# Kernel optimization log

Hardware: AMD Instinct MI355X
Metric: run time of the kernel (lower is better)

The kernel has to match this reference:

```python
import jax, jax.numpy as jnp
import numpy as np

B, T, C = 2, 2048, 1024
H, HS = 16, 64          # num_heads, head_size; H*HS == C
FF = 4 * C
EPS = 1e-5


def setup_inputs() -> dict:
    key = jax.random.key(0)
    ks = jax.random.split(key, 10)
    s = 0.02
    return {
        "x": jax.random.normal(ks[0], (B, T, C), dtype=jnp.float32),
        "Wq": jax.random.normal(ks[1], (H, C, HS), dtype=jnp.float32) * s,
        "Wk": jax.random.normal(ks[2], (H, C, HS), dtype=jnp.float32) * s,
        "Wv": jax.random.normal(ks[3], (H, C, HS), dtype=jnp.float32) * s,
        "p": jnp.ones((H,), dtype=jnp.float32),  # per-head learnable scale, init 1
        "Wproj": jax.random.normal(ks[4], (C, C), dtype=jnp.float32) * s,
        "W1": jax.random.normal(ks[5], (C, FF), dtype=jnp.float32) * s,
        "W2": jax.random.normal(ks[6], (FF, C), dtype=jnp.float32) * s,
        "ln1_w": jnp.ones((C,), dtype=jnp.float32),
        "ln1_b": jnp.zeros((C,), dtype=jnp.float32),
        "ln2_w": jnp.ones((C,), dtype=jnp.float32),
        "ln2_b": jnp.zeros((C,), dtype=jnp.float32),
    }


def _layernorm(x, w, b):
    mu = jnp.mean(x, axis=-1, keepdims=True)
    var = jnp.mean(jnp.square(x - mu), axis=-1, keepdims=True)
    return (x - mu) * jax.lax.rsqrt(var + EPS) * w + b


def reference(x, Wq, Wk, Wv, p, Wproj, W1, W2, ln1_w, ln1_b, ln2_w, ln2_b):
    # --- multi-head causal self-attention (dropout p=0 -> identity) ---
    h = _layernorm(x, ln1_w, ln1_b)
    q = jnp.einsum("btc,hcs->bhts", h, Wq)  # [B,H,T,HS]
    k = jnp.einsum("btc,hcs->bhts", h, Wk)
    v = jnp.einsum("btc,hcs->bhts", h, Wv)
    scale = p ** (-0.5)  # per-head scale, p init to 1
    wei = jnp.einsum("bhts,bhks->bhtk", q, k) * scale[None, :, None, None]
    causal = jnp.tril(jnp.ones((T, T), dtype=bool))
    wei = jnp.where(causal[None, None], wei, -jnp.inf)
    wei = jax.nn.softmax(wei, axis=-1)
    att = jnp.einsum("bhtk,bhks->bhts", wei, v)          # [B,H,T,HS]
    att = att.transpose(0, 2, 1, 3).reshape(B, T, C)     # concat heads
    sa = att @ Wproj
    x = x + sa
    # --- feed-forward (activation_id=0 -> ReLU) ---
    h2 = _layernorm(x, ln2_w, ln2_b)
    ff = jax.nn.relu(h2 @ W1) @ W2
    return x + ff
```

## Files before the change

### kernel.cpp

```cpp
#include <hip/hip_runtime.h>


typedef _Float16 f16;
typedef _Float16 f16x8 __attribute__((ext_vector_type(8)));
typedef _Float16 f16x4v __attribute__((ext_vector_type(4)));
typedef float f32x4 __attribute__((ext_vector_type(4)));

static constexpr int Tn = 2048;
static constexpr int Cn = 1024;
static constexpr int HSn = 64;

__device__ __forceinline__ void glds16(const f16* g, f16* l) {
    __builtin_amdgcn_global_load_lds((const __attribute__((address_space(1))) void*)g,
                                     (__attribute__((address_space(3))) void*)l,
                                     16, 0, 0);
}

#define VMCNT(N) asm volatile("s_waitcnt vmcnt(" #N ")" ::: "memory")
__device__ __forceinline__ void barrier_raw() {
    asm volatile("" ::: "memory");
    __builtin_amdgcn_s_barrier();
    asm volatile("" ::: "memory");
}

__device__ __forceinline__ unsigned cvt_pk_u32(float a, float b) {
    auto v = __builtin_amdgcn_cvt_pkrtz(a, b);
    union { __fp16 h2 __attribute__((ext_vector_type(2))); unsigned u; } c;
    c.h2 = v;
    return c.u;
}

__global__ __launch_bounds__(256) void ln_kernel(const float* __restrict__ x,
                                                 const float* __restrict__ w,
                                                 const float* __restrict__ b,
                                                 f16* __restrict__ out) {
    int row = blockIdx.x;
    const float* xr = x + (size_t)row * Cn;
    int tid = threadIdx.x, l = tid & 63, wv = tid >> 6;
    float4 v = *(const float4*)(xr + tid * 4);
    float s = v.x + v.y + v.z + v.w;
    float sq = v.x * v.x + v.y * v.y + v.z * v.z + v.w * v.w;
#pragma unroll
    for (int off = 32; off > 0; off >>= 1) {
        s += __shfl_down(s, off);
        sq += __shfl_down(sq, off);
    }
    __shared__ float red[8];
    if (l == 0) { red[wv] = s; red[wv + 4] = sq; }
    __syncthreads();
    float ts = red[0] + red[1] + red[2] + red[3];
    float tq = red[4] + red[5] + red[6] + red[7];
    float mean = ts * (1.0f / Cn);
    float var = tq * (1.0f / Cn) - mean * mean;
    float rstd = rsqrtf(var + 1e-5f);
    float4 wv4 = *(const float4*)(w + tid * 4);
    float4 bv4 = *(const float4*)(b + tid * 4);
    f16x4v o;
    o[0] = (f16)((v.x - mean) * rstd * wv4.x + bv4.x);
    o[1] = (f16)((v.y - mean) * rstd * wv4.y + bv4.y);
    o[2] = (f16)((v.z - mean) * rstd * wv4.z + bv4.z);
    o[3] = (f16)((v.w - mean) * rstd * wv4.w + bv4.w);
    *(f16x4v*)(out + (size_t)row * Cn + tid * 4) = o;
}

__global__ __launch_bounds__(256) void tr_cast_f32(const float* __restrict__ in, int irs,
                                                   f16* __restrict__ out, int ors) {
    __shared__ float tile[32][33];
    int r0 = blockIdx.x * 32, c0 = blockIdx.y * 32;
    int t = threadIdx.x;
    int rr = t >> 3, c4 = (t & 7) * 4;
    float4 v = *(const float4*)(in + (size_t)(r0 + rr) * irs + c0 + c4);
    tile[rr][c4] = v.x; tile[rr][c4 + 1] = v.y; tile[rr][c4 + 2] = v.z; tile[rr][c4 + 3] = v.w;
    __syncthreads();
    int cc = t >> 3, r4 = (t & 7) * 4;
    f16x4v o;
    o[0] = (f16)tile[r4][cc];
    o[1] = (f16)tile[r4 + 1][cc];
    o[2] = (f16)tile[r4 + 2][cc];
    o[3] = (f16)tile[r4 + 3][cc];
    *(f16x4v*)(out + (size_t)(c0 + cc) * ors + r0 + r4) = o;
}

__global__ __launch_bounds__(256) void tr_cast_qkv(const float* __restrict__ Wq,
                                                   const float* __restrict__ Wk,
                                                   const float* __restrict__ Wv,
                                                   f16* __restrict__ out) {
    int z = blockIdx.z;
    int qkv = z >> 4, h = z & 15;
    const float* in = (qkv == 0 ? Wq : qkv == 1 ? Wk : Wv) + (size_t)h * Cn * HSn;
    f16* o = out + (size_t)(qkv * Cn + h * HSn) * Cn;
    __shared__ float tile[32][33];
    int r0 = blockIdx.x * 32, c0 = blockIdx.y * 32;
    int t = threadIdx.x;
    int rr = t >> 3, c4 = (t & 7) * 4;
    float4 v = *(const float4*)(in + (size_t)(r0 + rr) * HSn + c0 + c4);
    tile[rr][c4] = v.x; tile[rr][c4 + 1] = v.y; tile[rr][c4 + 2] = v.z; tile[rr][c4 + 3] = v.w;
    __syncthreads();
    int cc = t >> 3, r4 = (t & 7) * 4;
    f16x4v ov;
    ov[0] = (f16)tile[r4][cc];
    ov[1] = (f16)tile[r4 + 1][cc];
    ov[2] = (f16)tile[r4 + 2][cc];
    ov[3] = (f16)tile[r4 + 3][cc];
    *(f16x4v*)(o + (size_t)(c0 + cc) * Cn + r0 + r4) = ov;
}

__global__ __launch_bounds__(256) void tr_vT(const f16* __restrict__ QKV, f16* __restrict__ vT) {
    int bh = blockIdx.z;
    int b = bh >> 4, h = bh & 15;
    const f16* in = QKV + (size_t)b * Tn * 3072 + 2048 + h * HSn;
    f16* out = vT + (size_t)bh * HSn * Tn;
    int r0 = blockIdx.x * 64;
    __shared__ __align__(16) f16 tile[64][72];
    int t = threadIdx.x;
#pragma unroll
    for (int i = 0; i < 2; i++) {
        int f = i * 256 + t;
        int rr = f >> 3, c8 = (f & 7) * 8;
        *(uint4*)(&tile[rr][c8]) = *(const uint4*)(in + (size_t)(r0 + rr) * 3072 + c8);
    }
    __syncthreads();
#pragma unroll
    for (int i = 0; i < 2; i++) {
        int f = i * 256 + t;
        int cc = f >> 3, r8 = (f & 7) * 8;
        union { f16 h[8]; uint4 v; } u;
#pragma unroll
        for (int j = 0; j < 8; j++) u.h[j] = tile[r8 + j][cc];
        *(uint4*)(out + (size_t)cc * Tn + r0 + r8) = u.v;
    }
}

template <int EPI>
__global__ __launch_bounds__(512, 2) void gemm8(const f16* __restrict__ A, const f16* __restrict__ Bt,
                                                f16* __restrict__ Cout, int M, int N, int K) {
    __shared__ __align__(16) f16 Abuf[4][8192];
    __shared__ __align__(16) f16 Bbuf[4][8192];
    int wg = blockIdx.x;
    int xcd = wg & 7, idx = wg >> 3;
    int bm = xcd * 2 + (idx & 1), bn = idx >> 1;
    int tid = threadIdx.x, l = tid & 63, w = tid >> 6;
    int wr = w >> 2, wc = w & 3;

    f32x4 acc[8][4];
#pragma unroll
    for (int m = 0; m < 8; m++)
#pragma unroll
        for (int n = 0; n < 4; n++) acc[m][n] = f32x4{0.f, 0.f, 0.f, 0.f};

    int l15 = l & 15;
    int lane_off = l15 * 32 + (((l >> 4) ^ ((l15 >> 1) & 3)) << 3);
    const f16* Afr = &Abuf[0][wr * 4096 + lane_off];
    const f16* Bfr = &Bbuf[0][(wc >> 1) * 4096 + (wc & 1) * 2048 + lane_off];

    int srow = w * 16 + (l >> 2);
    int schunk = (l & 3) ^ ((l >> 3) & 3);
    const f16* agp = A + (size_t)(bm * 256 + srow) * K + schunk * 8;
    const f16* bgp = Bt + (size_t)(bn * 256 + srow) * K + schunk * 8;
    const size_t rK = (size_t)128 * K;
    f16* dstA = &Abuf[0][w * 512];
    f16* dstB = &Bbuf[0][w * 512];

    auto stage = [&](int kt, int bf) {
        int k0 = kt * 32;
        glds16(agp + k0, dstA + bf * 8192);
        glds16(agp + rK + k0, dstA + bf * 8192 + 4096);
        glds16(bgp + k0, dstB + bf * 8192);
        glds16(bgp + rK + k0, dstB + bf * 8192 + 4096);
    };

    int NT = K >> 5;
    stage(0, 0);
    stage(1, 1);
    stage(2, 2);
    for (int t = 0; t < NT; ++t) {
        int cb = t & 3;
        VMCNT(8);
        barrier_raw();
        const f16* Ab = Afr + cb * 8192;
        const f16* Bb = Bfr + cb * 8192;
        f16x8 af[4], bf4[4];
#pragma unroll
        for (int m = 0; m < 4; m++) af[m] = *(const f16x8*)(Ab + m * 512);
#pragma unroll
        for (int n = 0; n < 4; n++) bf4[n] = *(const f16x8*)(Bb + n * 512);
        if (t + 3 < NT) stage(t + 3, (t + 3) & 3);
        __builtin_amdgcn_s_setprio(1);
#pragma unroll
        for (int m = 0; m < 4; m++)
#pragma unroll
            for (int n = 0; n < 4; n++)
                acc[m][n] = __builtin_amdgcn_mfma_f32_16x16x32_f16(af[m], bf4[n], acc[m][n], 0, 0, 0);
        __builtin_amdgcn_s_setprio(0);
        barrier_raw();
#pragma unroll
        for (int m = 0; m < 4; m++) af[m] = *(const f16x8*)(Ab + (m + 4) * 512);
        __builtin_amdgcn_s_setprio(1);
#pragma unroll
        for (int m = 0; m < 4; m++)
#pragma unroll
            for (int n = 0; n < 4; n++)
                acc[m + 4][n] = __builtin_amdgcn_mfma_f32_16x16x32_f16(af[m], bf4[n], acc[m + 4][n], 0, 0, 0);
        __builtin_amdgcn_s_setprio(0);
    }
    VMCNT(0);

    int row0 = bm * 256 + wr * 128 + (l >> 4) * 4;
    int col0 = bn * 256 + wc * 64 + (l & 15);
#pragma unroll
    for (int m = 0; m < 8; m++) {
#pragma unroll
        for (int n = 0; n < 4; n++) {
#pragma unroll
            for (int r = 0; r < 4; r++) {
                size_t idx = (size_t)(row0 + m * 16 + r) * N + (col0 + n * 16);
                float v = acc[m][n][r];
                if constexpr (EPI == 1) v = fmaxf(v, 0.f);
                Cout[idx] = (f16)v;
            }
        }
    }
}

__device__ __forceinline__ void l2_map(int& bm, int& bn) {
    int wg = blockIdx.y * 32 + blockIdx.x;
    int x = wg & 7, idx = wg >> 3;
    bm = x * 4 + (idx & 3);
    bn = idx >> 2;
}

template <int EPI>
__global__ __launch_bounds__(512) void gemm_ks(const f16* __restrict__ A, const f16* __restrict__ Bt,
                                               void* __restrict__ Cout, const float* __restrict__ resid,
                                               int M, int N, int K) {
    __shared__ __align__(16) char smem[98304];
    f16* As = (f16*)smem;
    f16* Bs = (f16*)(smem + 49152);
    int bm, bn;
    l2_map(bm, bn);
    int tid = threadIdx.x, l = tid & 63, w = tid >> 6;
    int grp = w >> 2, wl = w & 3;
    int wr = wl >> 1, wc = wl & 1;
    int Kh = K >> 1;
    int KT = Kh >> 5;

    f32x4 acc[4][4];
#pragma unroll
    for (int m = 0; m < 4; m++)
#pragma unroll
        for (int n = 0; n < 4; n++) acc[m][n] = f32x4{0.f, 0.f, 0.f, 0.f};

    int schunk = (l & 3) ^ ((l >> 3) & 3);
    const f16* agp = A + (size_t)(bm * 128 + wl * 16 + (l >> 2)) * K + grp * Kh + schunk * 8;
    const f16* bgp = Bt + (size_t)(bn * 128 + wl * 16 + (l >> 2)) * K + grp * Kh + schunk * 8;
    const size_t half = (size_t)64 * K;
    f16* Ab = As + grp * 12288;
    f16* Bb = Bs + grp * 12288;

    auto stage = [&](int kt, int bf) {
        size_t k0 = (size_t)kt * 32;
        glds16(agp + k0, Ab + bf * 4096 + wl * 512);
        glds16(agp + half + k0, Ab + bf * 4096 + 2048 + wl * 512);
        glds16(bgp + k0, Bb + bf * 4096 + wl * 512);
        glds16(bgp + half + k0, Bb + bf * 4096 + 2048 + wl * 512);
    };

    int l15 = l & 15;
    int rbase = (wr * 64 + l15) * 32 + (((l >> 4) ^ ((l15 >> 1) & 3)) << 3);
    int cbase = (wc * 64 + l15) * 32 + (((l >> 4) ^ ((l15 >> 1) & 3)) << 3);

    stage(0, 0);
    if (KT > 1) stage(1, 1);
    int nb = 2;
    for (int kt = 0; kt < KT; ++kt) {
        int cb = kt % 3;
        if (kt + 1 < KT) VMCNT(4);
        else VMCNT(0);
        barrier_raw();
        if (kt + 2 < KT) { stage(kt + 2, nb); nb = (nb == 2) ? 0 : nb + 1; }
        f16x8 af[4], bfr[4];
#pragma unroll
        for (int m = 0; m < 4; m++) af[m] = *(const f16x8*)(Ab + cb * 4096 + rbase + m * 512);
#pragma unroll
        for (int n = 0; n < 4; n++) bfr[n] = *(const f16x8*)(Bb + cb * 4096 + cbase + n * 512);
        __builtin_amdgcn_s_setprio(1);
#pragma unroll
        for (int m = 0; m < 4; m++)
#pragma unroll
            for (int n = 0; n < 4; n++)
                acc[m][n] = __builtin_amdgcn_mfma_f32_16x16x32_f16(af[m], bfr[n], acc[m][n], 0, 0, 0);
        __builtin_amdgcn_s_setprio(0);
    }
    __syncthreads();

    float* red = (float*)smem;
#pragma unroll
    for (int m = 0; m < 4; m++) {
        if (grp == 1) {
#pragma unroll
            for (int n = 0; n < 4; n++)
                *(f32x4*)(red + wl * 1280 + l * 20 + n * 4) = acc[m][n];
        }
        __syncthreads();
        if (grp == 0) {
#pragma unroll
            for (int n = 0; n < 4; n++)
                acc[m][n] += *(const f32x4*)(red + wl * 1280 + l * 20 + n * 4);
        }
        __syncthreads();
    }

    if (grp == 0) {
        int row0 = bm * 128 + wr * 64 + (l >> 4) * 4;
        int col0 = bn * 128 + wc * 64 + (l & 15);
#pragma unroll
        for (int m = 0; m < 4; m++) {
#pragma unroll
            for (int n = 0; n < 4; n++) {
#pragma unroll
                for (int r = 0; r < 4; r++) {
                    size_t idx = (size_t)(row0 + m * 16 + r) * N + (col0 + n * 16);
                    float v = acc[m][n][r];
                    if constexpr (EPI == 0) ((f16*)Cout)[idx] = (f16)v;
                    else if constexpr (EPI == 1) ((f16*)Cout)[idx] = (f16)fmaxf(v, 0.f);
                    else ((float*)Cout)[idx] = v + resid[idx];
                }
            }
        }
    }
}

__global__ __launch_bounds__(256) void attn_kernel(const f16* __restrict__ QKV,
                                                   const f16* __restrict__ vT,
                                                   const float* __restrict__ p,
                                                   f16* __restrict__ att) {
    int i = blockIdx.x;
    int bh = (i & 7) * 4 + ((i >> 3) & 3);
    int qt = 31 - (i >> 5);
    int b = bh >> 4, h = bh & 15;
    int tid = threadIdx.x, w = tid >> 6, l = tid & 63;
    float sc2 = rsqrtf(p[h]) * 1.44269504f;

    __shared__ __align__(16) f16 Ks[2][4096];
    __shared__ __align__(16) f16 Vs[2][4096];
    __shared__ __align__(16) f16 Ps[4][16 * 80];
    f16* Pw = &Ps[w][0];

    int srow0 = tid >> 3;
    int c0 = (tid & 7) ^ (srow0 & 7);
    const f16* Kg = QKV + (size_t)b * Tn * 3072 + 1024 + h * HSn;
    const f16* Vg = vT + (size_t)bh * HSn * Tn;
    const f16* Kg0 = Kg + (size_t)srow0 * 3072 + c0 * 8;
    const f16* Kg1 = Kg + (size_t)(srow0 + 32) * 3072 + c0 * 8;
    const f16* Vg0 = Vg + (size_t)srow0 * Tn + c0 * 8;
    const f16* Vg1 = Vg + (size_t)(srow0 + 32) * Tn + c0 * 8;
    int dl = w * 512 + l * 8;

    int foff[8];
#pragma unroll
    for (int n = 0; n < 4; n++)
#pragma unroll
        for (int ks = 0; ks < 2; ks++)
            foff[n * 2 + ks] = (n * 16 + (l & 15)) * 128 +
                               (((ks * 32 + (l >> 4) * 8) * 2) ^ ((l & 7) << 4));

    int qg = qt * 64 + w * 16 + (l & 15);
    int qo = qt * 64 + w * 16 + (l >> 4) * 4;
    const f16* qptr = QKV + (size_t)(b * Tn + qg) * 3072 + h * HSn + (l >> 4) * 8;
    f16x8 qf0 = *(const f16x8*)(qptr);
    f16x8 qf1 = *(const f16x8*)(qptr + 32);
    f16 sch = (f16)sc2;
#pragma unroll
    for (int j = 0; j < 8; j++) { qf0[j] *= sch; qf1[j] *= sch; }

    f32x4 o[4];
#pragma unroll
    for (int nf = 0; nf < 4; nf++) o[nf] = f32x4{0.f, 0.f, 0.f, 0.f};
    float m_r = -1e30f, l_r = 0.f;

    int nt = qt + 1;
    uint4 kr0 = *(const uint4*)(Kg0);
    uint4 kr1 = *(const uint4*)(Kg1);
    uint4 vr0 = *(const uint4*)(Vg0);
    uint4 vr1 = *(const uint4*)(Vg1);
    *(uint4*)(&Ks[0][dl]) = kr0;
    *(uint4*)(&Ks[0][2048 + dl]) = kr1;
    *(uint4*)(&Vs[0][dl]) = vr0;
    *(uint4*)(&Vs[0][2048 + dl]) = vr1;
    __syncthreads();
    for (int t = 0; t < nt; ++t) {
        int kv0 = t * 64;
        if (t + 1 < nt) {
            size_t ko = (size_t)(kv0 + 64) * 3072;
            kr0 = *(const uint4*)(Kg0 + ko);
            kr1 = *(const uint4*)(Kg1 + ko);
            vr0 = *(const uint4*)(Vg0 + kv0 + 64);
            vr1 = *(const uint4*)(Vg1 + kv0 + 64);
        }
        const char* Kb = (const char*)&Ks[t & 1][0];
        const char* Vb = (const char*)&Vs[t & 1][0];
        f32x4 s[4];
#pragma unroll
        for (int n = 0; n < 4; n++) s[n] = f32x4{0.f, 0.f, 0.f, 0.f};
        __builtin_amdgcn_s_setprio(1);
#pragma unroll
        for (int n = 0; n < 4; n++)
#pragma unroll
            for (int ks = 0; ks < 2; ks++) {
                f16x8 kf = *(const f16x8*)(Kb + foff[n * 2 + ks]);
                s[n] = __builtin_amdgcn_mfma_f32_16x16x32_f16(kf, ks == 0 ? qf0 : qf1, s[n], 0, 0, 0);
            }
        __builtin_amdgcn_s_setprio(0);
        if (t == qt) {
            int rel = qg - kv0;
#pragma unroll
            for (int n = 0; n < 4; n++)
#pragma unroll
                for (int r = 0; r < 4; r++) {
                    int kvr = n * 16 + (l >> 4) * 4 + r;
                    if (kvr > rel) s[n][r] = -1e30f;
                }
        }
        float tmax = -1e30f;
#pragma unroll
        for (int n = 0; n < 4; n++)
#pragma unroll
            for (int r = 0; r < 4; r++) tmax = fmaxf(tmax, s[n][r]);
        float lmul = 1.f;
        if (__any(tmax > m_r + 8.f)) {
            float rmax = fmaxf(tmax, __shfl_xor(tmax, 16));
            rmax = fmaxf(rmax, __shfl_xor(rmax, 32));
            float mnew = fmaxf(m_r, rmax);
            lmul = exp2f(m_r - mnew);
            m_r = mnew;
            float ar[4];
#pragma unroll
            for (int r = 0; r < 4; r++) ar[r] = __shfl(lmul, (l >> 4) * 4 + r);
#pragma unroll
            for (int nf = 0; nf < 4; nf++)
#pragma unroll
                for (int r = 0; r < 4; r++) o[nf][r] *= ar[r];
        }
        float rsum = 0.f;
#pragma unroll
        for (int n = 0; n < 4; n++) {
            float e0 = exp2f(s[n][0] - m_r), e1 = exp2f(s[n][1] - m_r);
            float e2 = exp2f(s[n][2] - m_r), e3 = exp2f(s[n][3] - m_r);
            rsum += (e0 + e1) + (e2 + e3);
            union { unsigned u[2]; f16x4v h4; } u;
            u.u[0] = cvt_pk_u32(e0, e1);
            u.u[1] = cvt_pk_u32(e2, e3);
            *(f16x4v*)(&Pw[(l & 15) * 80 + n * 16 + (l >> 4) * 4]) = u.h4;
        }
        l_r = l_r * lmul + rsum;
        f16x8 pa0 = *(const f16x8*)(&Pw[(l & 15) * 80 + (l >> 4) * 8]);
        f16x8 pa1 = *(const f16x8*)(&Pw[(l & 15) * 80 + 32 + (l >> 4) * 8]);
        __builtin_amdgcn_s_setprio(1);
#pragma unroll
        for (int nf = 0; nf < 4; nf++)
#pragma unroll
            for (int ks = 0; ks < 2; ks++) {
                f16x8 vf = *(const f16x8*)(Vb + foff[nf * 2 + ks]);
                o[nf] = __builtin_amdgcn_mfma_f32_16x16x32_f16(ks == 0 ? pa0 : pa1, vf, o[nf], 0, 0, 0);
            }
        __builtin_amdgcn_s_setprio(0);
        if (t + 1 < nt) {
            int nbf = (t + 1) & 1;
            *(uint4*)(&Ks[nbf][dl]) = kr0;
            *(uint4*)(&Ks[nbf][2048 + dl]) = kr1;
            *(uint4*)(&Vs[nbf][dl]) = vr0;
            *(uint4*)(&Vs[nbf][2048 + dl]) = vr1;
            __syncthreads();
        }
    }
    float lsum = l_r;
    lsum += __shfl_xor(lsum, 16);
    lsum += __shfl_xor(lsum, 32);
    float lro[4];
#pragma unroll
    for (int r = 0; r < 4; r++) lro[r] = __shfl(lsum, (l >> 4) * 4 + r);
#pragma unroll
    for (int nf = 0; nf < 4; nf++) {
#pragma unroll
        for (int r = 0; r < 4; r++) {
            float v = o[nf][r] / lro[r];
            att[(size_t)(b * Tn + qo + r) * Cn + h * HSn + nf * 16 + (l & 15)] = (f16)v;
        }
    }
}

extern "C" void kernel_launch(void* const* d_in, const int* in_sizes, int n_in,
                              void* d_out, int out_size, void* d_ws, size_t ws_size,
                              hipStream_t stream) {
    const float* x = (const float*)d_in[0];
    const float* Wq = (const float*)d_in[1];
    const float* Wk = (const float*)d_in[2];
    const float* Wv = (const float*)d_in[3];
    const float* p = (const float*)d_in[4];
    const float* Wproj = (const float*)d_in[5];
    const float* W1 = (const float*)d_in[6];
    const float* W2 = (const float*)d_in[7];
    const float* ln1w = (const float*)d_in[8];
    const float* ln1b = (const float*)d_in[9];
    const float* ln2w = (const float*)d_in[10];
    const float* ln2b = (const float*)d_in[11];

    char* ws = (char*)d_ws;
    const size_t MB = 1ull << 20;
    f16* Wqkv_t = (f16*)(ws + 0 * MB);
    f16* Wproj_t = (f16*)(ws + 6 * MB);
    f16* W1_t = (f16*)(ws + 8 * MB);
    f16* W2_t = (f16*)(ws + 16 * MB);
    float* x1 = (float*)(ws + 24 * MB);
    f16* QKV = (f16*)(ws + 40 * MB);
    f16* h1 = (f16*)(ws + 64 * MB);
    f16* vTb = (f16*)(ws + 64 * MB);
    f16* attb = (f16*)(ws + 72 * MB);
    f16* h2 = attb;
    f16* ffh = QKV;
    float* out = (float*)d_out;

    tr_cast_qkv<<<dim3(32, 2, 48), 256, 0, stream>>>(Wq, Wk, Wv, Wqkv_t);
    tr_cast_f32<<<dim3(32, 32), 256, 0, stream>>>(Wproj, 1024, Wproj_t, 1024);
    tr_cast_f32<<<dim3(32, 128), 256, 0, stream>>>(W1, 4096, W1_t, 1024);
    tr_cast_f32<<<dim3(128, 32), 256, 0, stream>>>(W2, 1024, W2_t, 4096);

    ln_kernel<<<4096, 256, 0, stream>>>(x, ln1w, ln1b, h1);
    gemm8<0><<<192, 512, 0, stream>>>(h1, Wqkv_t, QKV, 4096, 3072, 1024);
    tr_vT<<<dim3(32, 1, 32), 256, 0, stream>>>(QKV, vTb);
    attn_kernel<<<1024, 256, 0, stream>>>(QKV, vTb, p, attb);
    gemm_ks<2><<<dim3(32, 8), 512, 0, stream>>>(attb, Wproj_t, x1, x, 4096, 1024, 1024);
    ln_kernel<<<4096, 256, 0, stream>>>(x1, ln2w, ln2b, h2);
    gemm8<1><<<256, 512, 0, stream>>>(h2, W1_t, ffh, 4096, 4096, 1024);
    gemm_ks<2><<<dim3(32, 8), 512, 0, stream>>>(ffh, W2_t, out, x1, 4096, 1024, 4096);
}
```

Baseline: 216.8 us.

## Load B fragments directly from global in split-K GEMM, halving LDS use

The split-K projection and FF2 GEMM no longer stage B tiles through LDS. Each wave reads its B fragments straight from global memory into registers, and only A is triple-buffered in shared memory. LDS per block drops from 96KB to 48KB and launch bounds now request higher occupancy, aiming to remove LDS traffic and raise concurrency. The trade-off is redundant, less coalesced global/L2 reads of B across waves and more exposed global-load latency inside the k-loop. The removed KT>1 guard and the VMCNT placement inside the loop also change the synchronization assumptions.

```diff
diff --git a/kernel.cpp b/kernel.cpp
--- a/kernel.cpp
+++ b/kernel.cpp
@@ -230,12 +230,10 @@
 }
 
 template <int EPI>
-__global__ __launch_bounds__(512) void gemm_ks(const f16* __restrict__ A, const f16* __restrict__ Bt,
-                                               void* __restrict__ Cout, const float* __restrict__ resid,
-                                               int M, int N, int K) {
-    __shared__ __align__(16) char smem[98304];
-    f16* As = (f16*)smem;
-    f16* Bs = (f16*)(smem + 49152);
+__global__ __launch_bounds__(512, 4) void gemm_bd(const f16* __restrict__ A, const f16* __restrict__ Bt,
+                                                  void* __restrict__ Cout, const float* __restrict__ resid,
+                                                  int M, int N, int K) {
+    __shared__ __align__(16) f16 As[2][3][4096];
     int bm, bn;
     l2_map(bm, bn);
     int tid = threadIdx.x, l = tid & 63, w = tid >> 6;
@@ -252,37 +250,35 @@
 
     int schunk = (l & 3) ^ ((l >> 3) & 3);
     const f16* agp = A + (size_t)(bm * 128 + wl * 16 + (l >> 2)) * K + grp * Kh + schunk * 8;
-    const f16* bgp = Bt + (size_t)(bn * 128 + wl * 16 + (l >> 2)) * K + grp * Kh + schunk * 8;
     const size_t half = (size_t)64 * K;
-    f16* Ab = As + grp * 12288;
-    f16* Bb = Bs + grp * 12288;
+    f16* Ab = &As[grp][0][0];
 
     auto stage = [&](int kt, int bf) {
         size_t k0 = (size_t)kt * 32;
         glds16(agp + k0, Ab + bf * 4096 + wl * 512);
         glds16(agp + half + k0, Ab + bf * 4096 + 2048 + wl * 512);
-        glds16(bgp + k0, Bb + bf * 4096 + wl * 512);
-        glds16(bgp + half + k0, Bb + bf * 4096 + 2048 + wl * 512);
     };
 
     int l15 = l & 15;
     int rbase = (wr * 64 + l15) * 32 + (((l >> 4) ^ ((l15 >> 1) & 3)) << 3);
-    int cbase = (wc * 64 + l15) * 32 + (((l >> 4) ^ ((l15 >> 1) & 3)) << 3);
+    const f16* bgf = Bt + (size_t)(bn * 128 + wc * 64 + l15) * K + grp * Kh + (l >> 4) * 8;
 
     stage(0, 0);
-    if (KT > 1) stage(1, 1);
+    stage(1, 1);
+    VMCNT(2);
     int nb = 2;
     for (int kt = 0; kt < KT; ++kt) {
         int cb = kt % 3;
-        if (kt + 1 < KT) VMCNT(4);
-        else VMCNT(0);
         barrier_raw();
+        f16x8 bfr[4];
+#pragma unroll
+        for (int n = 0; n < 4; n++)
+            bfr[n] = *(const f16x8*)(bgf + (size_t)n * 16 * K + kt * 32);
+        asm volatile("" ::: "memory");
         if (kt + 2 < KT) { stage(kt + 2, nb); nb = (nb == 2) ? 0 : nb + 1; }
-        f16x8 af[4], bfr[4];
+        f16x8 af[4];
 #pragma unroll
         for (int m = 0; m < 4; m++) af[m] = *(const f16x8*)(Ab + cb * 4096 + rbase + m * 512);
-#pragma unroll
-        for (int n = 0; n < 4; n++) bfr[n] = *(const f16x8*)(Bb + cb * 4096 + cbase + n * 512);
         __builtin_amdgcn_s_setprio(1);
 #pragma unroll
         for (int m = 0; m < 4; m++)
@@ -293,7 +289,7 @@
     }
     __syncthreads();
 
-    float* red = (float*)smem;
+    float* red = (float*)&As[0][0][0];
 #pragma unroll
     for (int m = 0; m < 4; m++) {
         if (grp == 1) {
@@ -529,8 +525,8 @@
     gemm8<0><<<192, 512, 0, stream>>>(h1, Wqkv_t, QKV, 4096, 3072, 1024);
     tr_vT<<<dim3(32, 1, 32), 256, 0, stream>>>(QKV, vTb);
     attn_kernel<<<1024, 256, 0, stream>>>(QKV, vTb, p, attb);
-    gemm_ks<2><<<dim3(32, 8), 512, 0, stream>>>(attb, Wproj_t, x1, x, 4096, 1024, 1024);
+    gemm_bd<2><<<dim3(32, 8), 512, 0, stream>>>(attb, Wproj_t, x1, x, 4096, 1024, 1024);
     ln_kernel<<<4096, 256, 0, stream>>>(x1, ln2w, ln2b, h2);
     gemm8<1><<<256, 512, 0, stream>>>(h2, W1_t, ffh, 4096, 4096, 1024);
-    gemm_ks<2><<<dim3(32, 8), 512, 0, stream>>>(ffh, W2_t, out, x1, 4096, 1024, 4096);
-}
+    gemm_bd<2><<<dim3(32, 8), 512, 0, stream>>>(ffh, W2_t, out, x1, 4096, 1024, 4096);
+}
```

New measurement: 272.7 us. 25.8% more time.
